# Optimization experiments

Measured on AMD Instinct MI355X. Metric: run time of the kernel, lower is better.

The kernel has to match this reference:

```python
import jax, jax.numpy as jnp
import numpy as np

K = 32          # num_sets (experts)
D_IN = 10       # input_size
D_H = 20        # hidden_size
D_OUT = 1       # output_size
B = 262144      # batch


def setup_inputs() -> dict:
    key = jax.random.key(0)
    ks = jax.random.split(key, 6)
    # Kaiming-uniform-ish init scale like torch Linear defaults
    s1 = 1.0 / np.sqrt(D_IN)
    s2 = 1.0 / np.sqrt(D_H)
    return {
        "input_data": jax.random.normal(ks[0], (B, D_IN), dtype=jnp.float32),
        "W1": jax.random.uniform(ks[1], (K, D_H, D_IN), jnp.float32, -s1, s1),
        "b1": jax.random.uniform(ks[2], (K, D_H), jnp.float32, -s1, s1),
        "W2": jax.random.uniform(ks[3], (K, D_OUT, D_H), jnp.float32, -s2, s2),
        "b2": jax.random.uniform(ks[4], (K, D_OUT), jnp.float32, -s2, s2),
        "prototypes": jax.random.normal(ks[5], (K, D_IN), dtype=jnp.float32),
    }


def reference(input_data, W1, b1, W2, b2, prototypes):
    # All K tiny experts as one batched GEMM: [B,K,H]
    h = jax.nn.relu(jnp.einsum("bi,khi->bkh", input_data, W1) + b1[None])
    preds = jnp.einsum("bkh,koh->bko", h, W2) + b2[None]          # [B,K,O]
    # Distance-based softmax gating over experts
    diff = input_data[:, None, :] - prototypes[None, :, :]        # [B,K,D]
    dist = jnp.sqrt(jnp.sum(diff * diff, axis=2))                 # [B,K]
    attn = jax.nn.softmax(-dist, axis=1)                          # [B,K]
    return jnp.sum(preds * attn[:, :, None], axis=1)              # [B,O]
```

## Files before the change

### kernel.cpp

```cpp
#include <hip/hip_runtime.h>


#define KX 32
#define DIN 10
#define DH 20
#define BLOCK 512
#define WPB 8
#define TPW 2

typedef short bf16x8 __attribute__((ext_vector_type(8)));
typedef float f32x16 __attribute__((ext_vector_type(16)));
typedef float v2f    __attribute__((ext_vector_type(2)));

#define ZERO16 {0.f,0.f,0.f,0.f, 0.f,0.f,0.f,0.f, 0.f,0.f,0.f,0.f, 0.f,0.f,0.f,0.f}

__device__ inline unsigned short f2bf(float f) {
    unsigned int u = __float_as_uint(f);
    unsigned int r = u + 0x7fffu + ((u >> 16) & 1u);
    return (unsigned short)(r >> 16);
}

union BFU { bf16x8 v; unsigned short s[8]; };

__global__ __launch_bounds__(BLOCK, 4) void moe_kernel(
    const float* __restrict__ x,
    const float* __restrict__ W1,
    const float* __restrict__ b1,
    const float* __restrict__ W2,
    const float* __restrict__ b2,
    const float* __restrict__ proto,
    float* __restrict__ out,
    int B)
{
    __shared__ bf16x8 s_af[KX * 40];
    __shared__ float  s_w2[KX * 24];
    __shared__ bf16x8 s_pf[64];
    __shared__ float  s_pn2[32];

    const int tid = threadIdx.x;

    for (int idx = tid; idx < KX * 40; idx += BLOCK) {
        const int e = idx / 40, rem = idx - e * 40;
        const int ks = rem / 20, h = rem - ks * 20;
        BFU u;
#pragma unroll
        for (int j = 0; j < 8; ++j) {
            const int kk = ks * 8 + j;
            float v = 0.f;
            if (kk < DIN) v = W1[(e * DH + h) * DIN + kk];
            else if (kk == DIN) v = b1[e * DH + h];
            u.s[j] = f2bf(v);
        }
        s_af[idx] = u.v;
    }
    for (int idx = tid; idx < KX * 24; idx += BLOCK) {
        const int e = idx / 24, rem = idx - e * 24;
        const int hf = rem / 12, q = rem - hf * 12;
        float v = 0.f;
        if (q < 10) {
            const int m = (q & 3) + 8 * (q >> 2) + 4 * hf;
            const int h = (m & 3) + 4 * (m >> 3) + ((m & 4) ? 10 : 0);
            v = W2[e * DH + h];
        }
        s_w2[idx] = v;
    }
    if (tid < 64) {
        const int m = tid & 31, kb = (tid >> 5) * 8;
        BFU u;
#pragma unroll
        for (int j = 0; j < 8; ++j) {
            const int kk = kb + j;
            u.s[j] = f2bf(kk < DIN ? proto[m * DIN + kk] : 0.f);
        }
        s_pf[tid] = u.v;
    }
    if (tid < 32) {
        const int hf = tid >> 4, q = tid & 15;
        const int p = (q & 3) + 8 * (q >> 2) + 4 * hf;
        float s = 0.f;
#pragma unroll
        for (int i = 0; i < DIN; ++i) { const float v = proto[p * DIN + i]; s = fmaf(v, v, s); }
        s_pn2[tid] = s;
    }
    __syncthreads();

    const int lane = tid & 63;
    const int wave = tid >> 6;
    const int half = lane >> 5;
    const int col  = lane & 31;
    const bf16x8 pfrag = s_pf[lane];
    const f32x16 kZero = ZERO16;

    const int m = col;
    const bool mvalid = (m & 4) ? (m < 22) : (m < 18);
    const int hidx = (m & 3) + 4 * (m >> 3) + ((m & 4) ? 10 : 0);
    const int abase = half * 20 + (mvalid ? hidx : 0);

    int    row[TPW];
    bf16x8 xfrag[TPW];
    float  gate[TPW][16];
    float  nsum[TPW], dsum[TPW];

#pragma unroll
    for (int t = 0; t < TPW; ++t) {
        row[t] = ((blockIdx.x * WPB + wave) * TPW + t) * 32 + col;
        const int rr = (row[t] < B) ? row[t] : (B - 1);

        float xe[8];
        const float* xr = x + (size_t)rr * DIN;
        if (half == 0) {
#pragma unroll
            for (int i = 0; i < 4; ++i) {
                const float2 v = *(const float2*)(xr + 2 * i);
                xe[2 * i] = v.x; xe[2 * i + 1] = v.y;
            }
        } else {
            const float2 v = *(const float2*)(xr + 8);
            xe[0] = v.x; xe[1] = v.y; xe[2] = 1.f;
            xe[3] = 0.f; xe[4] = 0.f; xe[5] = 0.f; xe[6] = 0.f; xe[7] = 0.f;
        }
        BFU xu;
#pragma unroll
        for (int j = 0; j < 8; ++j) xu.s[j] = f2bf(xe[j]);
        xfrag[t] = xu.v;

        float part;
        if (half == 0) {
            part = 0.f;
#pragma unroll
            for (int j = 0; j < 8; ++j) part = fmaf(xe[j], xe[j], part);
        } else {
            part = fmaf(xe[0], xe[0], xe[1] * xe[1]);
        }
        const float xn2 = part + __shfl_xor(part, 32);

        const f32x16 dotg = __builtin_amdgcn_mfma_f32_32x32x16_bf16(pfrag, xfrag[t], kZero, 0, 0, 0);
        const float* pn2h = s_pn2 + half * 16;
        float ds = 0.f;
#pragma unroll
        for (int q = 0; q < 16; ++q) {
            float d2 = fmaf(dotg[q], -2.f, xn2 + pn2h[q]);
            d2 = fmaxf(d2, 0.f);
            const float g = __expf(-__fsqrt_rn(d2));
            gate[t][q] = g;
            ds += g;
        }
        dsum[t] = ds;
        nsum[t] = 0.f;
    }

#pragma unroll 2
    for (int j = 0; j < 16; ++j) {
        const int elo = (j & 3) + 8 * (j >> 2);
        const int ehi = elo + 4;

        bf16x8 alo = {0, 0, 0, 0, 0, 0, 0, 0};
        bf16x8 ahi = {0, 0, 0, 0, 0, 0, 0, 0};
        if (mvalid) {
            alo = s_af[elo * 40 + abase];
            ahi = s_af[ehi * 40 + abase];
        }
        const float4* w4lo = (const float4*)(s_w2 + elo * 24 + half * 12);
        const float4* w4hi = (const float4*)(s_w2 + ehi * 24 + half * 12);
        const float4 wl0 = w4lo[0], wl1 = w4lo[1], wl2 = w4lo[2];
        const float4 wh0 = w4hi[0], wh1 = w4hi[1], wh2 = w4hi[2];
        const float b2own = half ? b2[ehi] : b2[elo];

#pragma unroll
        for (int t = 0; t < TPW; ++t) {
            const f32x16 clo = __builtin_amdgcn_mfma_f32_32x32x16_bf16(alo, xfrag[t], kZero, 0, 0, 0);
            const f32x16 chi = __builtin_amdgcn_mfma_f32_32x32x16_bf16(ahi, xfrag[t], kZero, 0, 0, 0);

            v2f plov = v2f{0.f, 0.f}, phiv = v2f{0.f, 0.f};
            {
                v2f c;
                c = __builtin_elementwise_max(v2f{clo[0],  clo[1]},  v2f{0.f, 0.f});
                plov = __builtin_elementwise_fma(c, v2f{wl0.x, wl0.y}, plov);
                c = __builtin_elementwise_max(v2f{clo[2],  clo[3]},  v2f{0.f, 0.f});
                plov = __builtin_elementwise_fma(c, v2f{wl0.z, wl0.w}, plov);
                c = __builtin_elementwise_max(v2f{clo[4],  clo[5]},  v2f{0.f, 0.f});
                plov = __builtin_elementwise_fma(c, v2f{wl1.x, wl1.y}, plov);
                c = __builtin_elementwise_max(v2f{clo[6],  clo[7]},  v2f{0.f, 0.f});
                plov = __builtin_elementwise_fma(c, v2f{wl1.z, wl1.w}, plov);
                c = __builtin_elementwise_max(v2f{clo[8],  clo[9]},  v2f{0.f, 0.f});
                plov = __builtin_elementwise_fma(c, v2f{wl2.x, wl2.y}, plov);
                c = __builtin_elementwise_max(v2f{clo[10], clo[11]}, v2f{0.f, 0.f});
                plov = __builtin_elementwise_fma(c, v2f{wl2.z, wl2.w}, plov);

                c = __builtin_elementwise_max(v2f{chi[0],  chi[1]},  v2f{0.f, 0.f});
                phiv = __builtin_elementwise_fma(c, v2f{wh0.x, wh0.y}, phiv);
                c = __builtin_elementwise_max(v2f{chi[2],  chi[3]},  v2f{0.f, 0.f});
                phiv = __builtin_elementwise_fma(c, v2f{wh0.z, wh0.w}, phiv);
                c = __builtin_elementwise_max(v2f{chi[4],  chi[5]},  v2f{0.f, 0.f});
                phiv = __builtin_elementwise_fma(c, v2f{wh1.x, wh1.y}, phiv);
                c = __builtin_elementwise_max(v2f{chi[6],  chi[7]},  v2f{0.f, 0.f});
                phiv = __builtin_elementwise_fma(c, v2f{wh1.z, wh1.w}, phiv);
                c = __builtin_elementwise_max(v2f{chi[8],  chi[9]},  v2f{0.f, 0.f});
                phiv = __builtin_elementwise_fma(c, v2f{wh2.x, wh2.y}, phiv);
                c = __builtin_elementwise_max(v2f{chi[10], chi[11]}, v2f{0.f, 0.f});
                phiv = __builtin_elementwise_fma(c, v2f{wh2.z, wh2.w}, phiv);
            }
            const float pplo = plov.x + plov.y;
            const float pphi = phiv.x + phiv.y;

            const float mine   = half ? pphi : pplo;
            const float theirs = half ? pplo : pphi;
            const float recv   = __shfl_xor(theirs, 32);
            const float pred   = mine + recv + b2own;
            nsum[t] = fmaf(gate[t][j], pred, nsum[t]);
        }
    }

#pragma unroll
    for (int t = 0; t < TPW; ++t) {
        float ns = nsum[t] + __shfl_xor(nsum[t], 32);
        float ds = dsum[t] + __shfl_xor(dsum[t], 32);
        if (half == 0 && row[t] < B) out[row[t]] = ns / ds;
    }
}

extern "C" void kernel_launch(void* const* d_in, const int* in_sizes, int n_in,
                              void* d_out, int out_size, void* d_ws, size_t ws_size,
                              hipStream_t stream) {
    const float* x     = (const float*)d_in[0];
    const float* W1    = (const float*)d_in[1];
    const float* b1    = (const float*)d_in[2];
    const float* W2    = (const float*)d_in[3];
    const float* b2    = (const float*)d_in[4];
    const float* proto = (const float*)d_in[5];
    float* out = (float*)d_out;

    const int B = out_size;
    const int rows_per_block = WPB * TPW * 32;
    const int grid = (B + rows_per_block - 1) / rows_per_block;
    hipLaunchKernelGGL(moe_kernel, dim3(grid), dim3(BLOCK), 0, stream,
                       x, W1, b1, W2, b2, proto, out, B);
}
```

Before: 95.40 us.

## Reorganize expert MFMA to loop over hidden units with all experts per tile

The expert MLP is restructured so that each MFMA computes one hidden unit for all 32 experts at once. The A operand is W1 row jj across experts, and the second layer is accumulated per expert in registers across 20 hidden-unit iterations. This replaces 32 padded MFMAs (16 iterations of lo/hi pairs, with wasted hidden-slot rows) by 20 fully used MFMAs per tile. It also removes the per-iteration cross-half shuffle and the stored gate array. Gating is now computed after the loop and b2 is folded into a shared float2 table, at the cost of 16 live v2f accumulators per tile.

```diff
diff --git a/kernel.cpp b/kernel.cpp
--- a/kernel.cpp
+++ b/kernel.cpp
@@ -32,37 +32,32 @@
     float* __restrict__ out,
     int B)
 {
-    __shared__ bf16x8 s_af[KX * 40];
-    __shared__ float  s_w2[KX * 24];
+    __shared__ bf16x8 s_af2[DH * 64];
+    __shared__ __attribute__((aligned(16))) float s_w2c[DH * 32];
     __shared__ bf16x8 s_pf[64];
-    __shared__ float  s_pn2[32];
+    __shared__ float2 s_gk[32];
 
     const int tid = threadIdx.x;
 
-    for (int idx = tid; idx < KX * 40; idx += BLOCK) {
-        const int e = idx / 40, rem = idx - e * 40;
-        const int ks = rem / 20, h = rem - ks * 20;
+    for (int idx = tid; idx < DH * 64; idx += BLOCK) {
+        const int jj = idx >> 6, rem = idx & 63;
+        const int e = rem >> 1, ks = rem & 1;
         BFU u;
 #pragma unroll
         for (int j = 0; j < 8; ++j) {
             const int kk = ks * 8 + j;
             float v = 0.f;
-            if (kk < DIN) v = W1[(e * DH + h) * DIN + kk];
-            else if (kk == DIN) v = b1[e * DH + h];
+            if (kk < DIN) v = W1[(e * DH + jj) * DIN + kk];
+            else if (kk == DIN) v = b1[e * DH + jj];
             u.s[j] = f2bf(v);
         }
-        s_af[idx] = u.v;
-    }
-    for (int idx = tid; idx < KX * 24; idx += BLOCK) {
-        const int e = idx / 24, rem = idx - e * 24;
-        const int hf = rem / 12, q = rem - hf * 12;
-        float v = 0.f;
-        if (q < 10) {
-            const int m = (q & 3) + 8 * (q >> 2) + 4 * hf;
-            const int h = (m & 3) + 4 * (m >> 3) + ((m & 4) ? 10 : 0);
-            v = W2[e * DH + h];
-        }
-        s_w2[idx] = v;
+        s_af2[idx] = u.v;
+    }
+    for (int idx = tid; idx < DH * 32; idx += BLOCK) {
+        const int jj = idx >> 5, rem = idx & 31;
+        const int hf = rem >> 4, q = rem & 15;
+        const int p = (q & 3) + 8 * (q >> 2) + 4 * hf;
+        s_w2c[idx] = W2[p * DH + jj];
     }
     if (tid < 64) {
         const int m = tid & 31, kb = (tid >> 5) * 8;
@@ -80,7 +75,7 @@
         float s = 0.f;
 #pragma unroll
         for (int i = 0; i < DIN; ++i) { const float v = proto[p * DIN + i]; s = fmaf(v, v, s); }
-        s_pn2[tid] = s;
+        s_gk[tid] = make_float2(s, b2[p]);
     }
     __syncthreads();
 
@@ -90,16 +85,12 @@
     const int col  = lane & 31;
     const bf16x8 pfrag = s_pf[lane];
     const f32x16 kZero = ZERO16;
-
-    const int m = col;
-    const bool mvalid = (m & 4) ? (m < 22) : (m < 18);
-    const int hidx = (m & 3) + 4 * (m >> 3) + ((m & 4) ? 10 : 0);
-    const int abase = half * 20 + (mvalid ? hidx : 0);
+    const int aoff = (col << 1) + half;
 
     int    row[TPW];
     bf16x8 xfrag[TPW];
-    float  gate[TPW][16];
-    float  nsum[TPW], dsum[TPW];
+    float  xn2[TPW];
+    v2f    pa[TPW][8];
 
 #pragma unroll
     for (int t = 0; t < TPW; ++t) {
@@ -132,90 +123,61 @@
         } else {
             part = fmaf(xe[0], xe[0], xe[1] * xe[1]);
         }
-        const float xn2 = part + __shfl_xor(part, 32);
-
-        const f32x16 dotg = __builtin_amdgcn_mfma_f32_32x32x16_bf16(pfrag, xfrag[t], kZero, 0, 0, 0);
-        const float* pn2h = s_pn2 + half * 16;
-        float ds = 0.f;
+        xn2[t] = part + __shfl_xor(part, 32);
+
+#pragma unroll
+        for (int i = 0; i < 8; ++i) pa[t][i] = v2f{0.f, 0.f};
+    }
+
+    const float4* w2base = (const float4*)s_w2c + (half << 2);
+#pragma unroll 2
+    for (int jj = 0; jj < DH; ++jj) {
+        const bf16x8 a = s_af2[(jj << 6) + aoff];
+        const float4* w4 = w2base + (jj << 3);
+        const float4 w0 = w4[0], w1v = w4[1], w2v = w4[2], w3v = w4[3];
+
+#pragma unroll
+        for (int t = 0; t < TPW; ++t) {
+            const f32x16 c = __builtin_amdgcn_mfma_f32_32x32x16_bf16(a, xfrag[t], kZero, 0, 0, 0);
+            v2f r;
+            r = __builtin_elementwise_max(v2f{c[0],  c[1]},  v2f{0.f, 0.f});
+            pa[t][0] = __builtin_elementwise_fma(r, v2f{w0.x,  w0.y},  pa[t][0]);
+            r = __builtin_elementwise_max(v2f{c[2],  c[3]},  v2f{0.f, 0.f});
+            pa[t][1] = __builtin_elementwise_fma(r, v2f{w0.z,  w0.w},  pa[t][1]);
+            r = __builtin_elementwise_max(v2f{c[4],  c[5]},  v2f{0.f, 0.f});
+            pa[t][2] = __builtin_elementwise_fma(r, v2f{w1v.x, w1v.y}, pa[t][2]);
+            r = __builtin_elementwise_max(v2f{c[6],  c[7]},  v2f{0.f, 0.f});
+            pa[t][3] = __builtin_elementwise_fma(r, v2f{w1v.z, w1v.w}, pa[t][3]);
+            r = __builtin_elementwise_max(v2f{c[8],  c[9]},  v2f{0.f, 0.f});
+            pa[t][4] = __builtin_elementwise_fma(r, v2f{w2v.x, w2v.y}, pa[t][4]);
+            r = __builtin_elementwise_max(v2f{c[10], c[11]}, v2f{0.f, 0.f});
+            pa[t][5] = __builtin_elementwise_fma(r, v2f{w2v.z, w2v.w}, pa[t][5]);
+            r = __builtin_elementwise_max(v2f{c[12], c[13]}, v2f{0.f, 0.f});
+            pa[t][6] = __builtin_elementwise_fma(r, v2f{w3v.x, w3v.y}, pa[t][6]);
+            r = __builtin_elementwise_max(v2f{c[14], c[15]}, v2f{0.f, 0.f});
+            pa[t][7] = __builtin_elementwise_fma(r, v2f{w3v.z, w3v.w}, pa[t][7]);
+        }
+    }
+
+    const float2* gkh = s_gk + half * 16;
+#pragma unroll
+    for (int t = 0; t < TPW; ++t) {
+        const f32x16 dg = __builtin_amdgcn_mfma_f32_32x32x16_bf16(pfrag, xfrag[t], kZero, 0, 0, 0);
+        float ds = 0.f, ns = 0.f;
 #pragma unroll
         for (int q = 0; q < 16; ++q) {
-            float d2 = fmaf(dotg[q], -2.f, xn2 + pn2h[q]);
+            const float2 gk = gkh[q];
+            float d2 = fmaf(dg[q], -2.f, xn2[t] + gk.x);
             d2 = fmaxf(d2, 0.f);
             const float g = __expf(-__fsqrt_rn(d2));
-            gate[t][q] = g;
             ds += g;
-        }
-        dsum[t] = ds;
-        nsum[t] = 0.f;
-    }
-
-#pragma unroll 2
-    for (int j = 0; j < 16; ++j) {
-        const int elo = (j & 3) + 8 * (j >> 2);
-        const int ehi = elo + 4;
-
-        bf16x8 alo = {0, 0, 0, 0, 0, 0, 0, 0};
-        bf16x8 ahi = {0, 0, 0, 0, 0, 0, 0, 0};
-        if (mvalid) {
-            alo = s_af[elo * 40 + abase];
-            ahi = s_af[ehi * 40 + abase];
-        }
-        const float4* w4lo = (const float4*)(s_w2 + elo * 24 + half * 12);
-        const float4* w4hi = (const float4*)(s_w2 + ehi * 24 + half * 12);
-        const float4 wl0 = w4lo[0], wl1 = w4lo[1], wl2 = w4lo[2];
-        const float4 wh0 = w4hi[0], wh1 = w4hi[1], wh2 = w4hi[2];
-        const float b2own = half ? b2[ehi] : b2[elo];
-
-#pragma unroll
-        for (int t = 0; t < TPW; ++t) {
-            const f32x16 clo = __builtin_amdgcn_mfma_f32_32x32x16_bf16(alo, xfrag[t], kZero, 0, 0, 0);
-            const f32x16 chi = __builtin_amdgcn_mfma_f32_32x32x16_bf16(ahi, xfrag[t], kZero, 0, 0, 0);
-
-            v2f plov = v2f{0.f, 0.f}, phiv = v2f{0.f, 0.f};
-            {
-                v2f c;
-                c = __builtin_elementwise_max(v2f{clo[0],  clo[1]},  v2f{0.f, 0.f});
-                plov = __builtin_elementwise_fma(c, v2f{wl0.x, wl0.y}, plov);
-                c = __builtin_elementwise_max(v2f{clo[2],  clo[3]},  v2f{0.f, 0.f});
-                plov = __builtin_elementwise_fma(c, v2f{wl0.z, wl0.w}, plov);
-                c = __builtin_elementwise_max(v2f{clo[4],  clo[5]},  v2f{0.f, 0.f});
-                plov = __builtin_elementwise_fma(c, v2f{wl1.x, wl1.y}, plov);
-                c = __builtin_elementwise_max(v2f{clo[6],  clo[7]},  v2f{0.f, 0.f});
-                plov = __builtin_elementwise_fma(c, v2f{wl1.z, wl1.w}, plov);
-                c = __builtin_elementwise_max(v2f{clo[8],  clo[9]},  v2f{0.f, 0.f});
-                plov = __builtin_elementwise_fma(c, v2f{wl2.x, wl2.y}, plov);
-                c = __builtin_elementwise_max(v2f{clo[10], clo[11]}, v2f{0.f, 0.f});
-                plov = __builtin_elementwise_fma(c, v2f{wl2.z, wl2.w}, plov);
-
-                c = __builtin_elementwise_max(v2f{chi[0],  chi[1]},  v2f{0.f, 0.f});
-                phiv = __builtin_elementwise_fma(c, v2f{wh0.x, wh0.y}, phiv);
-                c = __builtin_elementwise_max(v2f{chi[2],  chi[3]},  v2f{0.f, 0.f});
-                phiv = __builtin_elementwise_fma(c, v2f{wh0.z, wh0.w}, phiv);
-                c = __builtin_elementwise_max(v2f{chi[4],  chi[5]},  v2f{0.f, 0.f});
-                phiv = __builtin_elementwise_fma(c, v2f{wh1.x, wh1.y}, phiv);
-                c = __builtin_elementwise_max(v2f{chi[6],  chi[7]},  v2f{0.f, 0.f});
-                phiv = __builtin_elementwise_fma(c, v2f{wh1.z, wh1.w}, phiv);
-                c = __builtin_elementwise_max(v2f{chi[8],  chi[9]},  v2f{0.f, 0.f});
-                phiv = __builtin_elementwise_fma(c, v2f{wh2.x, wh2.y}, phiv);
-                c = __builtin_elementwise_max(v2f{chi[10], chi[11]}, v2f{0.f, 0.f});
-                phiv = __builtin_elementwise_fma(c, v2f{wh2.z, wh2.w}, phiv);
-            }
-            const float pplo = plov.x + plov.y;
-            const float pphi = phiv.x + phiv.y;
-
-            const float mine   = half ? pphi : pplo;
-            const float theirs = half ? pplo : pphi;
-            const float recv   = __shfl_xor(theirs, 32);
-            const float pred   = mine + recv + b2own;
-            nsum[t] = fmaf(gate[t][j], pred, nsum[t]);
-        }
-    }
-
-#pragma unroll
-    for (int t = 0; t < TPW; ++t) {
-        float ns = nsum[t] + __shfl_xor(nsum[t], 32);
-        float ds = dsum[t] + __shfl_xor(dsum[t], 32);
-        if (half == 0 && row[t] < B) out[row[t]] = ns / ds;
+            const v2f pp = pa[t][q >> 1];
+            const float pq = (q & 1) ? pp.y : pp.x;
+            ns = fmaf(g, pq + gk.y, ns);
+        }
+        const float nst = ns + __shfl_xor(ns, 32);
+        const float dst = ds + __shfl_xor(ds, 32);
+        if (half == 0 && row[t] < B) out[row[t]] = nst / dst;
     }
 }
 
```

Measured after the change: 89.45 us. 1.07x faster.
